# Optimization experiments

Hardware: AMD Instinct MI355X
Metric: run time of the kernel (lower is better)

The kernel has to match this reference:

```python
import jax, jax.numpy as jnp
import numpy as np

EPS = 1e-6
NEG_INF = jnp.finfo(jnp.float32).min


def setup_inputs() -> dict:
    key = jax.random.key(0)
    ks = jax.random.split(key, 12)
    N, D, H, dh, F, V, L, B = 4, 1024, 16, 64, 4096, 32000, 2048, 1
    s = 0.02
    return {
        "x_BL": jax.random.randint(ks[0], (B, L), 0, V, dtype=jnp.int32),
        "embed": jax.random.normal(ks[1], (V, D), jnp.float32) * s,
        "pos_embed": jax.random.normal(ks[2], (L, D), jnp.float32) * s,
        "wq": jax.random.normal(ks[3], (N, D, H, dh), jnp.float32) * s,
        "wk": jax.random.normal(ks[4], (N, D, H, dh), jnp.float32) * s,
        "wv": jax.random.normal(ks[5], (N, D, H, dh), jnp.float32) * s,
        "wo": jax.random.normal(ks[6], (N, H, dh, D), jnp.float32) * s,
        "gate_w": jax.random.normal(ks[7], (N, D, F), jnp.float32) * s,
        "val_w": jax.random.normal(ks[8], (N, D, F), jnp.float32) * s,
        "ffn_out_w": jax.random.normal(ks[9], (N, F, D), jnp.float32) * s,
        "ln1_s": jnp.ones((N, D), jnp.float32),
        "ln2_s": jnp.ones((N, D), jnp.float32),
        "final_ln_s": jnp.ones((D,), jnp.float32),
    }


def rmsnorm(x, scale):
    var = jnp.mean(jnp.square(x), axis=-1, keepdims=True)
    return x * jax.lax.rsqrt(var + EPS) * scale


def attention(x_BLD, wq, wk, wv, wo):
    # wq/wk/wv: [D,H,dh]; wo: [H,dh,D]
    q = jnp.einsum('bld,dhk->blhk', x_BLD, wq)
    k = jnp.einsum('bld,dhk->blhk', x_BLD, wk)
    v = jnp.einsum('bld,dhk->blhk', x_BLD, wv)
    dh = wq.shape[-1]
    a = jnp.einsum('bqhd,bkhd->bhqk', q, k) / (dh ** 0.5)
    L = x_BLD.shape[1]
    mask = jnp.tril(jnp.ones((1, 1, L, L), dtype=jnp.bool_))
    a = jnp.where(mask, a, NEG_INF)
    a = jax.nn.softmax(a, axis=-1)
    o = jnp.einsum('bhqk,bkhd->bqhd', a, v)
    return jnp.einsum('bqhd,hdD->bqD', o, wo)


def ffn(x_BLD, gate_w, val_w, out_w):
    g = jax.nn.swish(jnp.einsum('bld,df->blf', x_BLD, gate_w))
    y = jnp.einsum('bld,df->blf', x_BLD, val_w) * g
    return jnp.einsum('blf,fd->bld', y, out_w)


def reference(x_BL, embed, pos_embed, wq, wk, wv, wo, gate_w, val_w,
              ffn_out_w, ln1_s, ln2_s, final_ln_s):
    x = embed[x_BL]                              # [B,L,D]
    L = x_BL.shape[1]
    x = x + pos_embed[jnp.arange(L)][None, :, :]
    N = wq.shape[0]
    for i in range(N):
        a = attention(rmsnorm(x, ln1_s[i]), wq[i], wk[i], wv[i], wo[i])
        f = ffn(rmsnorm(x, ln2_s[i]), gate_w[i], val_w[i], ffn_out_w[i])
        x = x + a + f
    x = rmsnorm(x, final_ln_s)
    logits = jnp.einsum('bld,vd->blv', x, embed)  # tied embedding attend
    return logits
```

## Files before the change

### kernel.cpp

```cpp
#include <hip/hip_runtime.h>
#include <cstdint>
#include <cstddef>

#define L_SEQ 2048
#define DMODEL 1024
#define NHEAD 16
#define DHEAD 64
#define FFN_F 4096
#define VOCAB 32000
#define NLAYER 4

typedef __attribute__((ext_vector_type(8))) short short8;
typedef __attribute__((ext_vector_type(4))) float f32x4;

__device__ __forceinline__ unsigned short f2bf(float f) {
  unsigned int u = __float_as_uint(f);
  u += 0x7fffu + ((u >> 16) & 1u);
  return (unsigned short)(u >> 16);
}
__device__ __forceinline__ float b2f(unsigned short h) {
  return __uint_as_float(((unsigned int)h) << 16);
}

__device__ __forceinline__ void glds16(const unsigned short* g, unsigned short* l) {
  __builtin_amdgcn_global_load_lds(
      (const __attribute__((address_space(1))) unsigned int*)g,
      (__attribute__((address_space(3))) unsigned int*)l, 16, 0, 0);
}

__device__ __forceinline__ float rmax16(float v) {
  v = fmaxf(v, __shfl_xor(v, 1));
  v = fmaxf(v, __shfl_xor(v, 2));
  v = fmaxf(v, __shfl_xor(v, 4));
  v = fmaxf(v, __shfl_xor(v, 8));
  return v;
}
__device__ __forceinline__ float rsum16(float v) {
  v += __shfl_xor(v, 1);
  v += __shfl_xor(v, 2);
  v += __shfl_xor(v, 4);
  v += __shfl_xor(v, 8);
  return v;
}

#define MFMA(ACC, AF, BF) \
  ACC = __builtin_amdgcn_mfma_f32_16x16x32_bf16(AF, BF, ACC, 0, 0, 0)

enum { E_F32 = 0, E_BF16 = 1, E_SWIGLU = 2, E_PART = 3 };

template <int EPI>
__global__ __launch_bounds__(512, 2) void gemm8p(
    const unsigned short* __restrict__ A, const unsigned short* __restrict__ B,
    void* __restrict__ Cg, int M, int N, int K, int lda, int ldb, int ldc,
    float alpha, int nby)
{
  const int nwg = gridDim.x;
  const int orig = blockIdx.x;
  const int q = nwg >> 3, r = nwg & 7;
  const int xcd = orig & 7, rest = orig >> 3;
  const int wgid = (xcd < r ? xcd * (q + 1) : r * (q + 1) + (xcd - r) * q) + rest;
  const int by = wgid % nby, bx = wgid / nby;
  const int mb = by * 256, nb = bx * 256;

  __shared__ __align__(16) unsigned short As_[2][256 * 64];
  __shared__ __align__(16) unsigned short Bs_[2][256 * 64];

  const int tid = threadIdx.x;
  const int lane = tid & 63;
  const int w = tid >> 6;
  const int wm = (w >> 2) * 128;
  const int wn = (w & 3) * 64;
  const int lr = lane & 15;
  const int lg = lane >> 4;
  const int srow = lane >> 3;
  const int scol = ((lane & 7) ^ srow) * 8;
  const int slot0 = (lg ^ (lr & 7)) * 8;
  const int slot1 = ((4 + lg) ^ (lr & 7)) * 8;

  f32x4 acc[8][4];
#pragma unroll
  for (int i = 0; i < 8; i++)
#pragma unroll
    for (int j = 0; j < 4; j++) acc[i][j] = (f32x4){0.f, 0.f, 0.f, 0.f};

  const unsigned short* Ab = A + (size_t)(mb + srow) * lda + scol;
  const unsigned short* Bb = B + (size_t)(nb + srow) * ldb + scol;

  auto stageA = [&](int t, int R) {
    const int s = t & 1, kb = t << 6;
#pragma unroll
    for (int c = 0; c < 2; c++) {
      int cid = w * 2 + c;
      int rb = ((cid >> 3) << 7) + R * 64 + ((cid & 7) << 3);
      glds16(Ab + (size_t)rb * lda + kb, &As_[s][rb * 64]);
    }
  };
  auto stageB = [&](int t, int R) {
    const int s = t & 1, kb = t << 6;
#pragma unroll
    for (int c = 0; c < 2; c++) {
      int cid = w * 2 + c;
      int rb = ((cid >> 2) << 6) + R * 32 + ((cid & 3) << 3);
      glds16(Bb + (size_t)rb * ldb + kb, &Bs_[s][rb * 64]);
    }
  };

  const int nk = K >> 6;
  stageA(0, 0); stageA(0, 1); stageB(0, 0); stageB(0, 1);
  stageA(1, 0); stageB(1, 0); stageB(1, 1);
  asm volatile("s_waitcnt vmcnt(6)" ::: "memory");
  __builtin_amdgcn_s_barrier();

  short8 a[4][2], b0[2][2], b1[2][2];
#pragma unroll
  for (int j = 0; j < 2; j++) {
    b0[j][0] = *(const short8*)&Bs_[0][(wn + j * 16 + lr) * 64 + slot0];
    b0[j][1] = *(const short8*)&Bs_[0][(wn + j * 16 + lr) * 64 + slot1];
  }

  for (int t = 0; t < nk; ++t) {
    const int s = t & 1;
    const unsigned short* Asb = &As_[s][0];
    const unsigned short* Bsb = &Bs_[s][0];

#pragma unroll
    for (int i = 0; i < 4; i++) {
      a[i][0] = *(const short8*)&Asb[(wm + i * 16 + lr) * 64 + slot0];
      a[i][1] = *(const short8*)&Asb[(wm + i * 16 + lr) * 64 + slot1];
    }
    if (t + 1 < nk) stageA(t + 1, 1);
    __builtin_amdgcn_s_barrier();
    __builtin_amdgcn_s_setprio(1);
#pragma unroll
    for (int kk = 0; kk < 2; kk++)
#pragma unroll
      for (int i = 0; i < 4; i++)
#pragma unroll
        for (int j = 0; j < 2; j++) MFMA(acc[i][j], a[i][kk], b0[j][kk]);
    __builtin_amdgcn_s_setprio(0);
    __builtin_amdgcn_s_barrier();

#pragma unroll
    for (int j = 0; j < 2; j++) {
      b1[j][0] = *(const short8*)&Bsb[(wn + 32 + j * 16 + lr) * 64 + slot0];
      b1[j][1] = *(const short8*)&Bsb[(wn + 32 + j * 16 + lr) * 64 + slot1];
    }
    if (t + 2 < nk) stageA(t + 2, 0);
    __builtin_amdgcn_s_barrier();
    __builtin_amdgcn_s_setprio(1);
#pragma unroll
    for (int kk = 0; kk < 2; kk++)
#pragma unroll
      for (int i = 0; i < 4; i++)
#pragma unroll
        for (int j = 0; j < 2; j++) MFMA(acc[i][2 + j], a[i][kk], b1[j][kk]);
    __builtin_amdgcn_s_setprio(0);
    __builtin_amdgcn_s_barrier();

#pragma unroll
    for (int i = 0; i < 4; i++) {
      a[i][0] = *(const short8*)&Asb[(wm + 64 + i * 16 + lr) * 64 + slot0];
      a[i][1] = *(const short8*)&Asb[(wm + 64 + i * 16 + lr) * 64 + slot1];
    }
    if (t + 2 < nk) stageB(t + 2, 0);
    __builtin_amdgcn_s_barrier();
    __builtin_amdgcn_s_setprio(1);
#pragma unroll
    for (int kk = 0; kk < 2; kk++)
#pragma unroll
      for (int i = 0; i < 4; i++)
#pragma unroll
        for (int j = 0; j < 2; j++) MFMA(acc[4 + i][2 + j], a[i][kk], b1[j][kk]);
    __builtin_amdgcn_s_setprio(0);
    __builtin_amdgcn_s_barrier();

    if (t + 2 < nk) stageB(t + 2, 1);
    __builtin_amdgcn_s_barrier();
    __builtin_amdgcn_s_setprio(1);
#pragma unroll
    for (int kk = 0; kk < 2; kk++)
#pragma unroll
      for (int i = 0; i < 4; i++)
#pragma unroll
        for (int j = 0; j < 2; j++) MFMA(acc[4 + i][j], a[i][kk], b0[j][kk]);
    __builtin_amdgcn_s_setprio(0);
    if (t + 2 < nk) {
      asm volatile("s_waitcnt vmcnt(6)" ::: "memory");
    } else {
      asm volatile("s_waitcnt vmcnt(0)" ::: "memory");
    }
    __builtin_amdgcn_s_barrier();
    if (t + 1 < nk) {
      const unsigned short* Bn = &Bs_[s ^ 1][0];
#pragma unroll
      for (int j = 0; j < 2; j++) {
        b0[j][0] = *(const short8*)&Bn[(wn + j * 16 + lr) * 64 + slot0];
        b0[j][1] = *(const short8*)&Bn[(wn + j * 16 + lr) * 64 + slot1];
      }
    }
  }

#pragma unroll
  for (int i = 0; i < 8; i++) {
#pragma unroll
    for (int j = 0; j < 4; j++) {
      int oc = nb + wn + 16 * j + lr;
#pragma unroll
      for (int r4 = 0; r4 < 4; r4++) {
        int orow = mb + wm + 16 * i + lg * 4 + r4;
        float v = acc[i][j][r4] * alpha;
        if (EPI == E_F32) {
          ((float*)Cg)[(size_t)orow * ldc + oc] = v;
        } else if (EPI == E_BF16) {
          ((unsigned short*)Cg)[(size_t)orow * ldc + oc] = f2bf(v);
        } else if (EPI == E_SWIGLU) {
          float other = __shfl_xor(v, 1);
          float g = (lane & 1) ? other : v;
          float vv = (lane & 1) ? v : other;
          float sw = g / (1.0f + expf(-g)) * vv;
          if (!(lane & 1))
            ((unsigned short*)Cg)[(size_t)orow * ldc + (oc >> 1)] = f2bf(sw);
        }
      }
    }
  }
}

template <int EPI>
__global__ __launch_bounds__(256) void gemm_fast(
    const unsigned short* __restrict__ A, const unsigned short* __restrict__ B,
    void* __restrict__ Cg, int M, int N, int K, int lda, int ldb, int ldc,
    float alpha, int nbx)
{
  const int nwg = gridDim.x;
  const int orig = blockIdx.x;
  const int q = nwg >> 3, r = nwg & 7;
  const int xcd = orig & 7, rest = orig >> 3;
  const int wgid = (xcd < r ? xcd * (q + 1) : r * (q + 1) + (xcd - r) * q) + rest;
  const int bx = wgid % nbx, by = wgid / nbx;
  const int mb = by * 128;
  const int nb = bx * 128;

  const int Keff = (EPI == E_PART) ? (K >> 1) : K;
  const int koff = (EPI == E_PART) ? blockIdx.z * Keff : 0;

  __shared__ __align__(16) unsigned short As[2][128 * 64];
  __shared__ __align__(16) unsigned short Bs[2][128 * 64];

  const int tid = threadIdx.x;
  const int lane = tid & 63;
  const int wave = tid >> 6;
  const int wm = (wave >> 1) * 64;
  const int wn = (wave & 1) * 64;
  const int lr = lane & 15;
  const int lg = lane >> 4;

  const int srow = lane >> 3;
  const int scol = ((lane & 7) ^ srow) * 8;

  f32x4 acc[4][4];
#pragma unroll
  for (int i = 0; i < 4; i++)
#pragma unroll
    for (int j = 0; j < 4; j++) acc[i][j] = (f32x4){0.f, 0.f, 0.f, 0.f};

  const unsigned short* Abase = A + (size_t)(mb + wave * 32 + srow) * lda + koff + scol;
  const unsigned short* Bbase = B + (size_t)(nb + wave * 32 + srow) * ldb + koff + scol;

  auto stage = [&](int kb, int b) {
#pragma unroll
    for (int c = 0; c < 4; c++)
      glds16(Abase + (size_t)(c * 8) * lda + kb, &As[b][(wave * 32 + c * 8) * 64]);
#pragma unroll
    for (int c = 0; c < 4; c++)
      glds16(Bbase + (size_t)(c * 8) * ldb + kb, &Bs[b][(wave * 32 + c * 8) * 64]);
  };

  stage(0, 0);
  __syncthreads();
  int cur = 0;
  const int nk = Keff >> 6;

  for (int t = 0; t < nk; ++t) {
    if (t + 1 < nk) stage((t + 1) << 6, cur ^ 1);

    short8 af[2][4], bfb[2][4];
#pragma unroll
    for (int h = 0; h < 2; h++) {
      const int swz = ((h * 4 + lg) ^ (lr & 7)) * 8;
#pragma unroll
      for (int i = 0; i < 4; i++) {
        af[h][i] = *(const short8*)&As[cur][(wm + 16 * i + lr) * 64 + swz];
        bfb[h][i] = *(const short8*)&Bs[cur][(wn + 16 * i + lr) * 64 + swz];
      }
    }
#pragma unroll
    for (int h = 0; h < 2; h++)
#pragma unroll
      for (int i = 0; i < 4; i++)
#pragma unroll
        for (int j = 0; j < 4; j++) MFMA(acc[i][j], af[h][i], bfb[h][j]);

    __syncthreads();
    cur ^= 1;
  }

#pragma unroll
  for (int i = 0; i < 4; i++) {
#pragma unroll
    for (int j = 0; j < 4; j++) {
      int oc = nb + wn + 16 * j + lr;
#pragma unroll
      for (int r4 = 0; r4 < 4; r4++) {
        int orow = mb + wm + 16 * i + lg * 4 + r4;
        float v = acc[i][j][r4] * alpha;
        if (EPI == E_F32) {
          ((float*)Cg)[(size_t)orow * ldc + oc] = v;
        } else if (EPI == E_BF16) {
          ((unsigned short*)Cg)[(size_t)orow * ldc + oc] = f2bf(v);
        } else {
          float* C = (float*)Cg + (size_t)blockIdx.z * ((size_t)L_SEQ * DMODEL);
          C[(size_t)orow * ldc + oc] = v;
        }
      }
    }
  }
}

__global__ __launch_bounds__(128) void flash_attn(
    const unsigned short* __restrict__ Qg, const unsigned short* __restrict__ Kg,
    const unsigned short* __restrict__ Vt, unsigned short* __restrict__ Og,
    int ldq, int ldo)
{
  const int bid = blockIdx.x;
  const int slot = bid & 255, ph = bid >> 8;
  const int h = slot >> 4;
  const int qs = slot & 15;
  const int qb = ph ? (31 - qs) : qs;

  const int tid = threadIdx.x;
  const int lane = tid & 63;
  const int w = tid >> 6;
  const int lr = lane & 15;
  const int lg = lane >> 4;

  __shared__ __align__(16) unsigned short KsL[2][64 * 64];
  __shared__ __align__(16) unsigned short VsL[2][64 * 64];
  __shared__ __align__(16) unsigned short Ps[2][32 * 64];

  const int srow = lane >> 3;
  const int scol = ((lane & 7) ^ srow) * 8;

  short8 qf[2][2];
#pragma unroll
  for (int i = 0; i < 2; i++)
#pragma unroll
    for (int kk = 0; kk < 2; kk++)
      qf[i][kk] = *(const short8*)(Qg +
          (size_t)(qb * 64 + w * 32 + i * 16 + lr) * ldq + h * 64 + kk * 32 + lg * 8);

  f32x4 acc_o[2][4];
  float m_st[2][4], l_st[2][4];
#pragma unroll
  for (int i = 0; i < 2; i++)
#pragma unroll
    for (int j = 0; j < 4; j++) acc_o[i][j] = (f32x4){0.f, 0.f, 0.f, 0.f};
#pragma unroll
  for (int i = 0; i < 2; i++)
#pragma unroll
    for (int r = 0; r < 4; r++) { m_st[i][r] = -1e30f; l_st[i][r] = 0.f; }

  const int ntiles = qb + 1;
  const int qmin = qb * 64 + w * 32;

  auto stage = [&](int t, int buf) {
#pragma unroll
    for (int c = 0; c < 4; c++) {
      int row = w * 32 + c * 8 + srow;
      glds16(Kg + (size_t)(t * 64 + row) * ldq + h * 64 + scol,
             &KsL[buf][row * 64]);
      glds16(Vt + (size_t)(h * 64 + row) * L_SEQ + t * 64 + scol,
             &VsL[buf][row * 64]);
    }
  };

  stage(0, 0);
  __syncthreads();
  int buf = 0;

  for (int t = 0; t < ntiles; t++) {
    if (t + 1 < ntiles) stage(t + 1, buf ^ 1);

    f32x4 sa[2][4];
#pragma unroll
    for (int i = 0; i < 2; i++)
#pragma unroll
      for (int j = 0; j < 4; j++) sa[i][j] = (f32x4){0.f, 0.f, 0.f, 0.f};
#pragma unroll
    for (int kk = 0; kk < 2; kk++) {
      short8 kf[4];
#pragma unroll
      for (int j = 0; j < 4; j++)
        kf[j] = *(const short8*)&KsL[buf][(j * 16 + lr) * 64 + ((kk * 4 + lg) ^ (lr & 7)) * 8];
#pragma unroll
      for (int i = 0; i < 2; i++)
#pragma unroll
        for (int j = 0; j < 4; j++) MFMA(sa[i][j], qf[i][kk], kf[j]);
    }

    const bool diag = (t * 64 + 63) > qmin;
#pragma unroll
    for (int i = 0; i < 2; i++)
#pragma unroll
      for (int j = 0; j < 4; j++)
#pragma unroll
        for (int r = 0; r < 4; r++) {
          float s = sa[i][j][r] * 0.125f;
          if (diag) {
            int kg = t * 64 + j * 16 + lr;
            int qg = qmin + i * 16 + lg * 4 + r;
            if (kg > qg) s = -1e30f;
          }
          sa[i][j][r] = s;
        }

    float fsc[2][4], mnew[2][4];
#pragma unroll
    for (int i = 0; i < 2; i++)
#pragma unroll
      for (int r = 0; r < 4; r++) {
        float mx = fmaxf(fmaxf(sa[i][0][r], sa[i][1][r]), fmaxf(sa[i][2][r], sa[i][3][r]));
        mx = rmax16(mx);
        float mn = fmaxf(m_st[i][r], mx);
        mnew[i][r] = mn;
        fsc[i][r] = __expf(m_st[i][r] - mn);
        m_st[i][r] = mn;
      }
#pragma unroll
    for (int i = 0; i < 2; i++)
#pragma unroll
      for (int r = 0; r < 4; r++) {
        float ls = 0.f;
#pragma unroll
        for (int j = 0; j < 4; j++) {
          float p = __expf(sa[i][j][r] - mnew[i][r]);
          sa[i][j][r] = p;
          ls += p;
        }
        ls = rsum16(ls);
        l_st[i][r] = l_st[i][r] * fsc[i][r] + ls;
      }
#pragma unroll
    for (int i = 0; i < 2; i++)
#pragma unroll
      for (int j = 0; j < 4; j++)
#pragma unroll
        for (int r = 0; r < 4; r++) acc_o[i][j][r] *= fsc[i][r];

#pragma unroll
    for (int i = 0; i < 2; i++)
#pragma unroll
      for (int j = 0; j < 4; j++)
#pragma unroll
        for (int r = 0; r < 4; r++) {
          int qrl = lg * 4 + r;
          int idx = (i * 16 + qrl) * 64 + (((j * 2 + (lr >> 3)) ^ (qrl & 7)) * 8) + (lr & 7);
          Ps[w][idx] = f2bf(sa[i][j][r]);
        }

#pragma unroll
    for (int kk = 0; kk < 2; kk++) {
      short8 pf[2], vf[4];
#pragma unroll
      for (int i = 0; i < 2; i++)
        pf[i] = *(const short8*)&Ps[w][(i * 16 + lr) * 64 + ((kk * 4 + lg) ^ (lr & 7)) * 8];
#pragma unroll
      for (int j = 0; j < 4; j++)
        vf[j] = *(const short8*)&VsL[buf][(j * 16 + lr) * 64 + ((kk * 4 + lg) ^ (lr & 7)) * 8];
#pragma unroll
      for (int i = 0; i < 2; i++)
#pragma unroll
        for (int j = 0; j < 4; j++) MFMA(acc_o[i][j], pf[i], vf[j]);
    }

    __syncthreads();
    buf ^= 1;
  }

  float inv[2][4];
#pragma unroll
  for (int i = 0; i < 2; i++)
#pragma unroll
    for (int r = 0; r < 4; r++) inv[i][r] = 1.0f / l_st[i][r];
#pragma unroll
  for (int i = 0; i < 2; i++)
#pragma unroll
    for (int j = 0; j < 4; j++)
#pragma unroll
      for (int r = 0; r < 4; r++) {
        size_t row = qmin + i * 16 + lg * 4 + r;
        Og[row * ldo + h * 64 + j * 16 + lr] = f2bf(acc_o[i][j][r] * inv[i][r]);
      }
}

__global__ __launch_bounds__(256) void rmsnorm_fold(
    const float* __restrict__ xin,
    const float* __restrict__ p1, const float* __restrict__ p2,
    unsigned short* __restrict__ o1, float* __restrict__ xout, int fold)
{
  int row = blockIdx.x;
  int tid = threadIdx.x;
  float v[4];
  float ss = 0.f;
#pragma unroll
  for (int i = 0; i < 4; i++) {
    size_t idx = (size_t)row * DMODEL + tid + 256 * i;
    float val = xin[idx];
    if (fold) {
      val += p1[idx] + p2[idx];
      xout[idx] = val;
    }
    v[i] = val;
    ss += val * val;
  }
#pragma unroll
  for (int o = 32; o > 0; o >>= 1) ss += __shfl_xor(ss, o);
  __shared__ float red[4];
  if ((tid & 63) == 0) red[tid >> 6] = ss;
  __syncthreads();
  ss = red[0] + red[1] + red[2] + red[3];
  float inv = rsqrtf(ss / DMODEL + 1e-6f);
#pragma unroll
  for (int i = 0; i < 4; i++) {
    size_t idx = (size_t)row * DMODEL + tid + 256 * i;
    o1[idx] = f2bf(v[i] * inv);
  }
}

__global__ __launch_bounds__(256) void prep_weights(
    const float* __restrict__ wq, const float* __restrict__ wk,
    const float* __restrict__ wv, const float* __restrict__ wo,
    const float* __restrict__ gw, const float* __restrict__ vw,
    const float* __restrict__ fw, const float* __restrict__ s1,
    const float* __restrict__ s2,
    unsigned short* __restrict__ qkvw, unsigned short* __restrict__ wft,
    unsigned short* __restrict__ gvt)
{
  __shared__ float t0[32][33], t1[32][33];
  int bid = blockIdx.x;
  int tx = threadIdx.x, ty = threadIdx.y;
  if (bid < 4096) {
    int j = bid >> 10, tile = bid & 1023;
    int c0 = (tile & 31) * 32, r0 = (tile >> 5) * 32;
    const float* src = j == 0 ? wq : j == 1 ? wk : j == 2 ? wv : wo;
#pragma unroll
    for (int k = 0; k < 32; k += 8)
      t0[ty + k][tx] = src[(size_t)(r0 + ty + k) * 1024 + c0 + tx];
    __syncthreads();
    if (j < 3) {
      unsigned short* dst = qkvw + (size_t)j * 1024 * 1024;
      float sc = s1[r0 + tx];
#pragma unroll
      for (int k = 0; k < 32; k += 8)
        dst[(size_t)(c0 + ty + k) * 1024 + r0 + tx] = f2bf(t0[tx][ty + k] * sc);
    } else {
#pragma unroll
      for (int k = 0; k < 32; k += 8)
        wft[(size_t)(c0 + ty + k) * 5120 + r0 + tx] = f2bf(t0[tx][ty + k]);
    }
  } else if (bid < 8192) {
    int tile = bid - 4096;
    int c0 = (tile & 31) * 32;
    int r0 = (tile >> 5) * 32;
#pragma unroll
    for (int k = 0; k < 32; k += 8)
      t0[ty + k][tx] = fw[(size_t)(r0 + ty + k) * 1024 + c0 + tx];
    __syncthreads();
#pragma unroll
    for (int k = 0; k < 32; k += 8)
      wft[(size_t)(c0 + ty + k) * 5120 + 1024 + r0 + tx] = f2bf(t0[tx][ty + k]);
  } else {
    int tile = bid - 8192;
    int c0 = (tile & 127) * 32;
    int d0 = (tile >> 7) * 32;
#pragma unroll
    for (int k = 0; k < 32; k += 8) {
      t0[ty + k][tx] = gw[(size_t)(d0 + ty + k) * 4096 + c0 + tx];
      t1[ty + k][tx] = vw[(size_t)(d0 + ty + k) * 4096 + c0 + tx];
    }
    __syncthreads();
    float sc = s2[d0 + tx];
#pragma unroll
    for (int k = 0; k < 32; k += 8) {
      gvt[(size_t)(2 * (c0 + ty + k)) * 1024 + d0 + tx] = f2bf(t0[tx][ty + k] * sc);
      gvt[(size_t)(2 * (c0 + ty + k) + 1) * 1024 + d0 + tx] = f2bf(t1[tx][ty + k] * sc);
    }
  }
}

__global__ __launch_bounds__(256) void transpose_act(
    const unsigned short* __restrict__ in, unsigned short* __restrict__ out,
    int ld_in, int ld_out)
{
  __shared__ float tile[32][33];
  int c0 = blockIdx.x * 32;
  int r0 = blockIdx.y * 32;
  int tx = threadIdx.x;
  int ty = threadIdx.y;
#pragma unroll
  for (int j = 0; j < 32; j += 8)
    tile[ty + j][tx] = b2f(in[(size_t)(r0 + ty + j) * ld_in + c0 + tx]);
  __syncthreads();
#pragma unroll
  for (int j = 0; j < 32; j += 8)
    out[(size_t)(c0 + ty + j) * ld_out + r0 + tx] = f2bf(tile[tx][ty + j]);
}

__global__ __launch_bounds__(256) void convert_embb(
    const float* __restrict__ in, const float* __restrict__ lnf,
    unsigned short* __restrict__ out, size_t n)
{
  size_t i = ((size_t)blockIdx.x * 256 + threadIdx.x) * 4;
  if (i + 3 < n) {
    float4 v = *(const float4*)(in + i);
    int d = (int)(i & 1023);
    out[i] = f2bf(v.x * lnf[d]);
    out[i + 1] = f2bf(v.y * lnf[d + 1]);
    out[i + 2] = f2bf(v.z * lnf[d + 2]);
    out[i + 3] = f2bf(v.w * lnf[d + 3]);
  }
}

__global__ __launch_bounds__(256) void embed_kernel(
    const int* __restrict__ ids, const float* __restrict__ emb,
    const float* __restrict__ pos, float* __restrict__ x)
{
  int l = blockIdx.x;
  int id = ids[l];
#pragma unroll
  for (int i = 0; i < 4; i++) {
    int d = threadIdx.x + 256 * i;
    x[(size_t)l * DMODEL + d] = emb[(size_t)id * DMODEL + d] + pos[(size_t)l * DMODEL + d];
  }
}

extern "C" void kernel_launch(void* const* d_in, const int* in_sizes, int n_in,
                              void* d_out, int out_size, void* d_ws, size_t ws_size,
                              hipStream_t stream)
{
  const int L = L_SEQ, D = DMODEL, F = FFN_F, V = VOCAB;
  const int* ids = (const int*)d_in[0];
  const float* embed = (const float*)d_in[1];
  const float* pos = (const float*)d_in[2];
  const float* wq = (const float*)d_in[3];
  const float* wk = (const float*)d_in[4];
  const float* wv = (const float*)d_in[5];
  const float* wo = (const float*)d_in[6];
  const float* gatew = (const float*)d_in[7];
  const float* valw = (const float*)d_in[8];
  const float* ffow = (const float*)d_in[9];
  const float* ln1 = (const float*)d_in[10];
  const float* ln2 = (const float*)d_in[11];
  const float* lnf = (const float*)d_in[12];

  char* ws = (char*)d_ws;
  size_t off = 0;
  auto alloc = [&](size_t bytes) -> void* {
    void* p = ws + off;
    off += (bytes + 255) & ~(size_t)255;
    return p;
  };
  float* x = (float*)alloc((size_t)L * D * 4);
  float* pbuf = (float*)alloc((size_t)2 * L * D * 4);
  unsigned short* xhat = (unsigned short*)alloc((size_t)L * D * 2);
  unsigned short* qkvb = (unsigned short*)alloc((size_t)L * 3 * D * 2);
  unsigned short* vtb = (unsigned short*)alloc((size_t)L * D * 2);
  unsigned short* ohb = (unsigned short*)alloc((size_t)L * 5120 * 2);
  unsigned short* qkvw = (unsigned short*)alloc((size_t)3 * D * D * 2);
  unsigned short* gvt = (unsigned short*)alloc((size_t)2 * F * D * 2);
  unsigned short* wft = (unsigned short*)alloc((size_t)D * 5120 * 2);
  unsigned short* embb = (unsigned short*)alloc((size_t)V * D * 2);

  dim3 blk(256);
  dim3 blk512(512);
  dim3 blkT(32, 8);

  embed_kernel<<<L, blk, 0, stream>>>(ids, embed, pos, x);
  convert_embb<<<(unsigned)((size_t)V * D / 1024), blk, 0, stream>>>(
      embed, lnf, embb, (size_t)V * D);

  for (int i = 0; i < NLAYER; i++) {
    prep_weights<<<12288, blkT, 0, stream>>>(
        wq + (size_t)i * D * D, wk + (size_t)i * D * D, wv + (size_t)i * D * D,
        wo + (size_t)i * D * D, gatew + (size_t)i * D * F, valw + (size_t)i * D * F,
        ffow + (size_t)i * F * D, ln1 + (size_t)i * D, ln2 + (size_t)i * D,
        qkvw, wft, gvt);

    rmsnorm_fold<<<L, blk, 0, stream>>>(x, pbuf, pbuf + (size_t)L * D,
                                        xhat, x, i > 0 ? 1 : 0);

    gemm_fast<E_BF16><<<dim3(24 * 16), blk, 0, stream>>>(
        xhat, qkvw, qkvb, L, 3 * D, D, D, D, 3 * D, 1.0f, 24);

    transpose_act<<<dim3(D / 32, L / 32), blkT, 0, stream>>>(qkvb + 2 * D, vtb, 3 * D, L);

    flash_attn<<<dim3(512), dim3(128), 0, stream>>>(qkvb, qkvb + D, vtb, ohb, 3 * D, 5120);

    gemm8p<E_SWIGLU><<<dim3(8 * 32), blk512, 0, stream>>>(
        xhat, gvt, ohb + 1024, L, 2 * F, D, D, D, 5120, 1.0f, 8);

    gemm_fast<E_PART><<<dim3(8 * 16, 1, 2), blk, 0, stream>>>(
        ohb, wft, pbuf, L, D, 5120, 5120, 5120, D, 1.0f, 8);
  }

  rmsnorm_fold<<<L, blk, 0, stream>>>(x, pbuf, pbuf + (size_t)L * D,
                                      xhat, x, 1);
  gemm8p<E_F32><<<dim3(8 * 125), blk512, 0, stream>>>(
      xhat, embb, d_out, L, V, D, D, D, V, 1.0f, 8);
}
```

Before: 1.178 ms.

## Fuse V transpose into QKV GEMM epilogue, embed into rmsnorm, batch weight prep

The QKV GEMM now writes Q and K row-major into a narrower buffer and writes V directly transposed, so the separate transpose kernel goes away. The embedding lookup is folded into the first rmsnorm, which is also vectorized with float4 loads and stores. All layers' weight conversion is merged into one large launch before the layer loop, so per-layer prep launches disappear, at the cost of a larger workspace. The transposed V store from the GEMM epilogue is strided and uncoalesced, which could make that epilogue more expensive.

```diff
diff --git a/kernel.cpp b/kernel.cpp
--- a/kernel.cpp
+++ b/kernel.cpp
@@ -46,7 +46,7 @@
 #define MFMA(ACC, AF, BF) \
   ACC = __builtin_amdgcn_mfma_f32_16x16x32_bf16(AF, BF, ACC, 0, 0, 0)
 
-enum { E_F32 = 0, E_BF16 = 1, E_SWIGLU = 2, E_PART = 3 };
+enum { E_F32 = 0, E_BF16 = 1, E_SWIGLU = 2, E_PART = 3, E_QKVT = 4 };
 
 template <int EPI>
 __global__ __launch_bounds__(512, 2) void gemm8p(
@@ -229,7 +229,8 @@
 template <int EPI>
 __global__ __launch_bounds__(256) void gemm_fast(
     const unsigned short* __restrict__ A, const unsigned short* __restrict__ B,
-    void* __restrict__ Cg, int M, int N, int K, int lda, int ldb, int ldc,
+    void* __restrict__ Cg, void* __restrict__ Cg2,
+    int M, int N, int K, int lda, int ldb, int ldc,
     float alpha, int nbx)
 {
   const int nwg = gridDim.x;
@@ -318,6 +319,11 @@
           ((float*)Cg)[(size_t)orow * ldc + oc] = v;
         } else if (EPI == E_BF16) {
           ((unsigned short*)Cg)[(size_t)orow * ldc + oc] = f2bf(v);
+        } else if (EPI == E_QKVT) {
+          if (oc < 2048)
+            ((unsigned short*)Cg)[(size_t)orow * 2048 + oc] = f2bf(v);
+          else
+            ((unsigned short*)Cg2)[(size_t)(oc - 2048) * L_SEQ + orow] = f2bf(v);
         } else {
           float* C = (float*)Cg + (size_t)blockIdx.z * ((size_t)L_SEQ * DMODEL);
           C[(size_t)orow * ldc + oc] = v;
@@ -506,23 +512,31 @@
 __global__ __launch_bounds__(256) void rmsnorm_fold(
     const float* __restrict__ xin,
     const float* __restrict__ p1, const float* __restrict__ p2,
-    unsigned short* __restrict__ o1, float* __restrict__ xout, int fold)
+    const int* __restrict__ ids, const float* __restrict__ emb,
+    const float* __restrict__ pos,
+    unsigned short* __restrict__ o1, float* __restrict__ xout, int mode)
 {
   int row = blockIdx.x;
   int tid = threadIdx.x;
-  float v[4];
-  float ss = 0.f;
-#pragma unroll
-  for (int i = 0; i < 4; i++) {
-    size_t idx = (size_t)row * DMODEL + tid + 256 * i;
-    float val = xin[idx];
-    if (fold) {
-      val += p1[idx] + p2[idx];
-      xout[idx] = val;
-    }
-    v[i] = val;
-    ss += val * val;
-  }
+  size_t base = (size_t)row * DMODEL + tid * 4;
+  float4 val;
+  if (mode == 2) {
+    int id = ids[row];
+    float4 e = *(const float4*)(emb + (size_t)id * DMODEL + tid * 4);
+    float4 p = *(const float4*)(pos + base);
+    val.x = e.x + p.x; val.y = e.y + p.y; val.z = e.z + p.z; val.w = e.w + p.w;
+    *(float4*)(xout + base) = val;
+  } else if (mode == 1) {
+    float4 a = *(const float4*)(xin + base);
+    float4 b = *(const float4*)(p1 + base);
+    float4 c = *(const float4*)(p2 + base);
+    val.x = a.x + b.x + c.x; val.y = a.y + b.y + c.y;
+    val.z = a.z + b.z + c.z; val.w = a.w + b.w + c.w;
+    *(float4*)(xout + base) = val;
+  } else {
+    val = *(const float4*)(xin + base);
+  }
+  float ss = val.x * val.x + val.y * val.y + val.z * val.z + val.w * val.w;
 #pragma unroll
   for (int o = 32; o > 0; o >>= 1) ss += __shfl_xor(ss, o);
   __shared__ float red[4];
@@ -530,25 +544,38 @@
   __syncthreads();
   ss = red[0] + red[1] + red[2] + red[3];
   float inv = rsqrtf(ss / DMODEL + 1e-6f);
-#pragma unroll
-  for (int i = 0; i < 4; i++) {
-    size_t idx = (size_t)row * DMODEL + tid + 256 * i;
-    o1[idx] = f2bf(v[i] * inv);
-  }
-}
-
-__global__ __launch_bounds__(256) void prep_weights(
-    const float* __restrict__ wq, const float* __restrict__ wk,
-    const float* __restrict__ wv, const float* __restrict__ wo,
-    const float* __restrict__ gw, const float* __restrict__ vw,
-    const float* __restrict__ fw, const float* __restrict__ s1,
-    const float* __restrict__ s2,
-    unsigned short* __restrict__ qkvw, unsigned short* __restrict__ wft,
-    unsigned short* __restrict__ gvt)
+  ushort4 o;
+  o.x = f2bf(val.x * inv); o.y = f2bf(val.y * inv);
+  o.z = f2bf(val.z * inv); o.w = f2bf(val.w * inv);
+  *(ushort4*)(o1 + base) = o;
+}
+
+__global__ __launch_bounds__(256) void prep_weights_all(
+    const float* __restrict__ wq_, const float* __restrict__ wk_,
+    const float* __restrict__ wv_, const float* __restrict__ wo_,
+    const float* __restrict__ gw_, const float* __restrict__ vw_,
+    const float* __restrict__ fw_, const float* __restrict__ ln1_,
+    const float* __restrict__ ln2_,
+    unsigned short* __restrict__ qkvw_, unsigned short* __restrict__ wft_,
+    unsigned short* __restrict__ gvt_)
 {
   __shared__ float t0[32][33], t1[32][33];
-  int bid = blockIdx.x;
+  const int li = blockIdx.x / 12288;
+  int bid = blockIdx.x % 12288;
   int tx = threadIdx.x, ty = threadIdx.y;
+  const float* wq = wq_ + (size_t)li * 1024 * 1024;
+  const float* wk = wk_ + (size_t)li * 1024 * 1024;
+  const float* wv = wv_ + (size_t)li * 1024 * 1024;
+  const float* wo = wo_ + (size_t)li * 1024 * 1024;
+  const float* gw = gw_ + (size_t)li * 1024 * 4096;
+  const float* vw = vw_ + (size_t)li * 1024 * 4096;
+  const float* fw = fw_ + (size_t)li * 4096 * 1024;
+  const float* s1 = ln1_ + (size_t)li * 1024;
+  const float* s2 = ln2_ + (size_t)li * 1024;
+  unsigned short* qkvw = qkvw_ + (size_t)li * 3 * 1024 * 1024;
+  unsigned short* wft = wft_ + (size_t)li * 1024 * 5120;
+  unsigned short* gvt = gvt_ + (size_t)li * 2 * 4096 * 1024;
+
   if (bid < 4096) {
     int j = bid >> 10, tile = bid & 1023;
     int c0 = (tile & 31) * 32, r0 = (tile >> 5) * 32;
@@ -596,24 +623,6 @@
       gvt[(size_t)(2 * (c0 + ty + k) + 1) * 1024 + d0 + tx] = f2bf(t1[tx][ty + k] * sc);
     }
   }
-}
-
-__global__ __launch_bounds__(256) void transpose_act(
-    const unsigned short* __restrict__ in, unsigned short* __restrict__ out,
-    int ld_in, int ld_out)
-{
-  __shared__ float tile[32][33];
-  int c0 = blockIdx.x * 32;
-  int r0 = blockIdx.y * 32;
-  int tx = threadIdx.x;
-  int ty = threadIdx.y;
-#pragma unroll
-  for (int j = 0; j < 32; j += 8)
-    tile[ty + j][tx] = b2f(in[(size_t)(r0 + ty + j) * ld_in + c0 + tx]);
-  __syncthreads();
-#pragma unroll
-  for (int j = 0; j < 32; j += 8)
-    out[(size_t)(c0 + ty + j) * ld_out + r0 + tx] = f2bf(tile[tx][ty + j]);
 }
 
 __global__ __launch_bounds__(256) void convert_embb(
@@ -628,19 +637,6 @@
     out[i + 1] = f2bf(v.y * lnf[d + 1]);
     out[i + 2] = f2bf(v.z * lnf[d + 2]);
     out[i + 3] = f2bf(v.w * lnf[d + 3]);
-  }
-}
-
-__global__ __launch_bounds__(256) void embed_kernel(
-    const int* __restrict__ ids, const float* __restrict__ emb,
-    const float* __restrict__ pos, float* __restrict__ x)
-{
-  int l = blockIdx.x;
-  int id = ids[l];
-#pragma unroll
-  for (int i = 0; i < 4; i++) {
-    int d = threadIdx.x + 256 * i;
-    x[(size_t)l * DMODEL + d] = emb[(size_t)id * DMODEL + d] + pos[(size_t)l * DMODEL + d];
   }
 }
 
@@ -673,48 +669,47 @@
   float* x = (float*)alloc((size_t)L * D * 4);
   float* pbuf = (float*)alloc((size_t)2 * L * D * 4);
   unsigned short* xhat = (unsigned short*)alloc((size_t)L * D * 2);
-  unsigned short* qkvb = (unsigned short*)alloc((size_t)L * 3 * D * 2);
+  unsigned short* qkvb = (unsigned short*)alloc((size_t)L * 2 * D * 2);
   unsigned short* vtb = (unsigned short*)alloc((size_t)L * D * 2);
   unsigned short* ohb = (unsigned short*)alloc((size_t)L * 5120 * 2);
-  unsigned short* qkvw = (unsigned short*)alloc((size_t)3 * D * D * 2);
-  unsigned short* gvt = (unsigned short*)alloc((size_t)2 * F * D * 2);
-  unsigned short* wft = (unsigned short*)alloc((size_t)D * 5120 * 2);
+  unsigned short* qkvw = (unsigned short*)alloc((size_t)NLAYER * 3 * D * D * 2);
+  unsigned short* gvt = (unsigned short*)alloc((size_t)NLAYER * 2 * F * D * 2);
+  unsigned short* wft = (unsigned short*)alloc((size_t)NLAYER * D * 5120 * 2);
   unsigned short* embb = (unsigned short*)alloc((size_t)V * D * 2);
 
   dim3 blk(256);
   dim3 blk512(512);
   dim3 blkT(32, 8);
 
-  embed_kernel<<<L, blk, 0, stream>>>(ids, embed, pos, x);
   convert_embb<<<(unsigned)((size_t)V * D / 1024), blk, 0, stream>>>(
       embed, lnf, embb, (size_t)V * D);
+  prep_weights_all<<<NLAYER * 12288, blkT, 0, stream>>>(
+      wq, wk, wv, wo, gatew, valw, ffow, ln1, ln2, qkvw, wft, gvt);
 
   for (int i = 0; i < NLAYER; i++) {
-    prep_weights<<<12288, blkT, 0, stream>>>(
-        wq + (size_t)i * D * D, wk + (size_t)i * D * D, wv + (size_t)i * D * D,
-        wo + (size_t)i * D * D, gatew + (size_t)i * D * F, valw + (size_t)i * D * F,
-        ffow + (size_t)i * F * D, ln1 + (size_t)i * D, ln2 + (size_t)i * D,
-        qkvw, wft, gvt);
-
-    rmsnorm_fold<<<L, blk, 0, stream>>>(x, pbuf, pbuf + (size_t)L * D,
-                                        xhat, x, i > 0 ? 1 : 0);
-
-    gemm_fast<E_BF16><<<dim3(24 * 16), blk, 0, stream>>>(
-        xhat, qkvw, qkvb, L, 3 * D, D, D, D, 3 * D, 1.0f, 24);
-
-    transpose_act<<<dim3(D / 32, L / 32), blkT, 0, stream>>>(qkvb + 2 * D, vtb, 3 * D, L);
-
-    flash_attn<<<dim3(512), dim3(128), 0, stream>>>(qkvb, qkvb + D, vtb, ohb, 3 * D, 5120);
+    unsigned short* qkvw_l = qkvw + (size_t)i * 3 * D * D;
+    unsigned short* gvt_l = gvt + (size_t)i * 2 * F * D;
+    unsigned short* wft_l = wft + (size_t)i * D * 5120;
+
+    rmsnorm_fold<<<L, blk, 0, stream>>>(
+        i == 0 ? nullptr : x, pbuf, pbuf + (size_t)L * D,
+        ids, embed, pos, xhat, x, i == 0 ? 2 : 1);
+
+    gemm_fast<E_QKVT><<<dim3(24 * 16), blk, 0, stream>>>(
+        xhat, qkvw_l, qkvb, vtb, L, 3 * D, D, D, D, 2 * D, 1.0f, 24);
+
+    flash_attn<<<dim3(512), dim3(128), 0, stream>>>(
+        qkvb, qkvb + D, vtb, ohb, 2 * D, 5120);
 
     gemm8p<E_SWIGLU><<<dim3(8 * 32), blk512, 0, stream>>>(
-        xhat, gvt, ohb + 1024, L, 2 * F, D, D, D, 5120, 1.0f, 8);
+        xhat, gvt_l, ohb + 1024, L, 2 * F, D, D, D, 5120, 1.0f, 8);
 
     gemm_fast<E_PART><<<dim3(8 * 16, 1, 2), blk, 0, stream>>>(
-        ohb, wft, pbuf, L, D, 5120, 5120, 5120, D, 1.0f, 8);
+        ohb, wft_l, pbuf, nullptr, L, D, 5120, 5120, 5120, D, 1.0f, 8);
   }
 
   rmsnorm_fold<<<L, blk, 0, stream>>>(x, pbuf, pbuf + (size_t)L * D,
-                                      xhat, x, 1);
+                                      ids, embed, pos, xhat, x, 1);
   gemm8p<E_F32><<<dim3(8 * 125), blk512, 0, stream>>>(
       xhat, embb, d_out, L, V, D, D, D, V, 1.0f, 8);
 }
```

Result: slower. 1.241 ms (+5.4%).
